# Optimization experiments

Measured on AMD Instinct MI355X. Metric: run time of the kernel, lower is better.

Reference implementation:

```python
import jax, jax.numpy as jnp
import numpy as np

N_ATOMS = 50000
N_EDGES = 400000
N_MOL = 500
HID = 128
NRBF = 20
NLAYERS = 4
N_TYPES = 100
CUTOFF = 5.0


def _xavier(key, fi, fo):
    lim = float(np.sqrt(6.0 / (fi + fo)))
    return jax.random.uniform(key, (fi, fo), minval=-lim, maxval=lim, dtype=jnp.float32)


def setup_inputs() -> dict:
    key = jax.random.key(0)
    ks = jax.random.split(key, 8)
    z = jax.random.randint(ks[0], (N_ATOMS,), 0, N_TYPES)
    pos = jax.random.normal(ks[1], (N_ATOMS, 3), dtype=jnp.float32) * 3.0
    # ensure every node receives at least one message (row covers all nodes)
    row = jnp.concatenate([jnp.arange(N_ATOMS),
                           jax.random.randint(ks[2], (N_EDGES - N_ATOMS,), 0, N_ATOMS)])
    col = jax.random.randint(ks[3], (N_EDGES,), 0, N_ATOMS)
    edge_index = jnp.stack([row, col])
    batch = jnp.sort(jax.random.randint(ks[4], (N_ATOMS,), 0, N_MOL))
    emb = jax.random.normal(ks[5], (N_TYPES, HID), dtype=jnp.float32) * 0.1
    kk = iter(jax.random.split(ks[6], 4 * NLAYERS + 4))
    filt_W1 = jnp.stack([_xavier(next(kk), NRBF, HID) for _ in range(NLAYERS)])
    filt_W2 = jnp.stack([_xavier(next(kk), HID, 3 * HID) for _ in range(NLAYERS)])
    upd_W1 = jnp.stack([_xavier(next(kk), 3 * HID, HID) for _ in range(NLAYERS)])
    upd_W2 = jnp.stack([_xavier(next(kk), HID, 3 * HID) for _ in range(NLAYERS)])
    filt_b1 = jnp.zeros((NLAYERS, HID)); filt_b2 = jnp.zeros((NLAYERS, 3 * HID))
    upd_b1 = jnp.zeros((NLAYERS, HID)); upd_b2 = jnp.zeros((NLAYERS, 3 * HID))
    lam_W1 = _xavier(next(kk), HID, HID); lam_b1 = jnp.zeros((HID,))
    lam_W2 = _xavier(next(kk), HID, 1); lam_b2 = jnp.zeros((1,))
    phi_W1 = _xavier(next(kk), HID, HID); phi_b1 = jnp.zeros((HID,))
    phi_W2 = _xavier(next(kk), HID, 1); phi_b2 = jnp.zeros((1,))
    return dict(z=z, pos=pos, edge_index=edge_index, batch=batch, emb=emb,
                filt_W1=filt_W1, filt_b1=filt_b1, filt_W2=filt_W2, filt_b2=filt_b2,
                upd_W1=upd_W1, upd_b1=upd_b1, upd_W2=upd_W2, upd_b2=upd_b2,
                lam_W1=lam_W1, lam_b1=lam_b1, lam_W2=lam_W2, lam_b2=lam_b2,
                phi_W1=phi_W1, phi_b1=phi_b1, phi_W2=phi_W2, phi_b2=phi_b2)


def reference(z, pos, edge_index, batch, emb,
              filt_W1, filt_b1, filt_W2, filt_b2,
              upd_W1, upd_b1, upd_W2, upd_b2,
              lam_W1, lam_b1, lam_W2, lam_b2,
              phi_W1, phi_b1, phi_W2, phi_b2):
    row, col = edge_index[0], edge_index[1]
    diff = pos[col] - pos[row]                      # (E,3)
    dist = jnp.linalg.norm(diff, axis=1)            # (E,)
    dirs = diff / (dist[:, None] + 1e-8)            # (E,3)
    centers = jnp.linspace(0.0, CUTOFF, NRBF)
    rbf = jnp.exp(-(dist[:, None] - centers) ** 2)  # gamma=1 buffer, (E,NRBF)

    s = emb[z]                                      # (N,H)
    v = jnp.zeros((s.shape[0], HID, 3), dtype=s.dtype)

    for i in range(NLAYERS):
        h = jax.nn.silu(rbf @ filt_W1[i] + filt_b1[i]) @ filt_W2[i] + filt_b2[i]
        phi_ss, phi_vv, phi_sv = jnp.split(h, 3, axis=-1)   # (E,H) each
        s_col = s[col]                                       # (E,H)
        m_s = phi_ss * s_col                                 # (E,H)
        m_v = phi_vv[..., None] * v[col] + (phi_sv * s_col)[..., None] * dirs[:, None, :]  # (E,H,3)
        m_s = jax.ops.segment_sum(m_s, row, num_segments=N_ATOMS)
        m_v = jax.ops.segment_sum(m_v, row, num_segments=N_ATOMS)
        v_norm = jnp.linalg.norm(m_v, axis=-1)               # (N,H)
        u = jax.nn.silu(jnp.concatenate([s, m_s, v_norm], axis=-1) @ upd_W1[i] + upd_b1[i]) @ upd_W2[i] + upd_b2[i]
        delta_s, alpha, beta = jnp.split(u, 3, axis=-1)
        s = s + delta_s
        v = alpha[..., None] * v + beta[..., None] * m_v

    h_mol = jax.ops.segment_sum(s, batch, num_segments=N_MOL)
    counts = jax.ops.segment_sum(jnp.ones((N_ATOMS,), s.dtype), batch, num_segments=N_MOL)
    h_mol = h_mol / counts[:, None]
    lam = (jax.nn.silu(h_mol @ lam_W1 + lam_b1) @ lam_W2 + lam_b2)[:, 0]
    phi = jax.nn.sigmoid(jax.nn.silu(h_mol @ phi_W1 + phi_b1) @ phi_W2 + phi_b2)[:, 0]
    return lam, phi
```

## Files before the change

kernel.cpp:

```cpp
#include <hip/hip_runtime.h>
#include <hip/hip_bf16.h>

static constexpr int NA = 50000;
static constexpr int NE = 400000;
static constexpr int HD = 128;
static constexpr int NL = 4;
static constexpr int NM = 500;
static constexpr int EPB = 32;
static constexpr int HSW = 194;

typedef __hip_bfloat16 bf16;
typedef short short8 __attribute__((ext_vector_type(8)));
typedef float float4v __attribute__((ext_vector_type(4)));

__device__ __forceinline__ unsigned short f2bf_bits(float x) {
    union { float f; unsigned int u; } c; c.f = x;
    unsigned int lsb = (c.u >> 16) & 1u;
    return (unsigned short)((c.u + 0x7fffu + lsb) >> 16);
}
__device__ __forceinline__ float bf2f(unsigned short b) {
    union { unsigned int u; float f; } c; c.u = ((unsigned int)b) << 16;
    return c.f;
}
__device__ __forceinline__ float lo16f(unsigned int u) {
    union { unsigned int x; float f; } c; c.x = u << 16; return c.f;
}
__device__ __forceinline__ float hi16f(unsigned int u) {
    union { unsigned int x; float f; } c; c.x = u & 0xffff0000u; return c.f;
}
__device__ __forceinline__ float silu_f(float x) {
    float sg = 1.0f / (1.0f + __expf(-x));
    return x * sg;
}

__global__ void geom_kernel(const float* __restrict__ pos,
                            const int* __restrict__ row, const int* __restrict__ col,
                            float* __restrict__ dist_g, float* __restrict__ dirs) {
    int e = blockIdx.x * 256 + threadIdx.x;
    if (e >= NE) return;
    int r = row[e], c = col[e];
    float dx = pos[c*3+0] - pos[r*3+0];
    float dy = pos[c*3+1] - pos[r*3+1];
    float dz = pos[c*3+2] - pos[r*3+2];
    float dist = sqrtf(dx*dx + dy*dy + dz*dz);
    float inv = 1.0f / (dist + 1e-8f);
    dist_g[e] = dist;
    dirs[e*3+0] = dx*inv; dirs[e*3+1] = dy*inv; dirs[e*3+2] = dz*inv;
}

__global__ void deg_kernel(const int* __restrict__ row, int* __restrict__ deg) {
    int e = blockIdx.x * 256 + threadIdx.x;
    if (e >= NE) return;
    atomicAdd(&deg[row[e]], 1);
}

__global__ __launch_bounds__(1024) void blockscan_kernel(const int* __restrict__ deg,
                                                         int* __restrict__ incl,
                                                         int* __restrict__ btot) {
    __shared__ int sh[1024];
    int t = threadIdx.x;
    int i = blockIdx.x * 1024 + t;
    int x = (i < NA) ? deg[i] : 0;
    sh[t] = x;
    __syncthreads();
    for (int off = 1; off < 1024; off <<= 1) {
        int v_ = (t >= off) ? sh[t - off] : 0;
        __syncthreads();
        sh[t] += v_;
        __syncthreads();
    }
    if (i < NA) incl[i] = sh[t];
    if (t == 1023) btot[blockIdx.x] = sh[t];
}

__global__ void totals_kernel(int* __restrict__ btot, int nb) {
    if (threadIdx.x == 0 && blockIdx.x == 0) {
        int acc = 0;
        for (int b = 0; b < nb; ++b) { int tv = btot[b]; btot[b] = acc; acc += tv; }
    }
}

__global__ void finalize_kernel(const int* __restrict__ deg, const int* __restrict__ incl,
                                const int* __restrict__ btot,
                                int* __restrict__ row_ptr, int* __restrict__ cursor) {
    int i = blockIdx.x * 256 + threadIdx.x;
    if (i >= NA) return;
    int inc = btot[i >> 10] + incl[i];
    row_ptr[i + 1] = inc;
    cursor[i] = inc - deg[i];
    if (i == 0) row_ptr[0] = 0;
}

__global__ void scatter_kernel(const int* __restrict__ row, int* __restrict__ cursor,
                               int* __restrict__ csr_eid) {
    int e = blockIdx.x * 256 + threadIdx.x;
    if (e >= NE) return;
    int p = atomicAdd(&cursor[row[e]], 1);
    csr_eid[p] = e;
}

__global__ void embed_kernel(const int* __restrict__ z, const float* __restrict__ emb,
                             float* __restrict__ s, uint4* __restrict__ vp2) {
    int idx = blockIdx.x * 256 + threadIdx.x;
    if (idx >= NA * 64) return;
    int n = idx >> 6, cp = idx & 63;
    float vlo = emb[z[n] * HD + cp];
    float vhi = emb[z[n] * HD + 64 + cp];
    s[(size_t)n * HD + cp] = vlo;
    s[(size_t)n * HD + 64 + cp] = vhi;
    uint4 q;
    q.x = (unsigned int)f2bf_bits(vlo);
    q.y = 0u;
    q.z = (unsigned int)f2bf_bits(vhi);
    q.w = 0u;
    vp2[idx] = q;
}

__global__ void pack_bfrag_kernel(const float* __restrict__ W, int K, int N,
                                  int layers, unsigned short* __restrict__ out) {
    int NT = N >> 4, KC = K >> 5;
    int total = layers * NT * KC * 64;
    int idx = blockIdx.x * 256 + threadIdx.x;
    if (idx >= total) return;
    int lane = idx & 63;
    int kc = (idx >> 6) % KC;
    int nt = ((idx >> 6) / KC) % NT;
    int layer = (idx >> 6) / (KC * NT);
    const float* Wl = W + (size_t)layer * K * N;
    int n = nt * 16 + (lane & 15);
    int k0 = kc * 32 + (lane >> 4) * 8;
    short8 pk;
#pragma unroll
    for (int j = 0; j < 8; ++j)
        pk[j] = (short)f2bf_bits(Wl[(size_t)(k0 + j) * N + n]);
    *(short8*)(&out[(size_t)idx * 8]) = pk;
}

__global__ void pack_w1frag_kernel(const float* __restrict__ W1all,
                                   unsigned short* __restrict__ out) {
    int idx = blockIdx.x * 256 + threadIdx.x;
    if (idx >= NL * 8 * 64) return;
    int lane = idx & 63;
    int nt = (idx >> 6) & 7;
    int layer = idx >> 9;
    const float* W1 = W1all + (size_t)layer * 20 * HD;
    int n = nt * 16 + (lane & 15);
    int k0 = (lane >> 4) * 8;
    short8 pk;
#pragma unroll
    for (int j = 0; j < 8; ++j) {
        int k = k0 + j;
        pk[j] = (k < 20) ? (short)f2bf_bits(W1[(size_t)k * HD + n]) : (short)0;
    }
    *(short8*)(&out[(size_t)idx * 8]) = pk;
}

__global__ __launch_bounds__(256, 6) void layer_msg_kernel(
    const float* __restrict__ dist_g, const int* __restrict__ csr_eid,
    const int* __restrict__ row_ptr, const int* __restrict__ row,
    const int* __restrict__ col, const float* __restrict__ dirs,
    const unsigned short* __restrict__ W1frag, const float* __restrict__ b1,
    const unsigned short* __restrict__ W2frag, const float* __restrict__ b2,
    const uint4* __restrict__ vp2,
    float* __restrict__ m_s, float* __restrict__ m_v)
{
    __shared__ __align__(16) unsigned int smem32[EPB * HSW];
    unsigned short* t_frag = (unsigned short*)smem32;
    __shared__ float dist_s[EPB];
    __shared__ int   col_s[EPB];
    __shared__ int   rid_s[EPB];
    __shared__ float dirs_s[EPB * 3];

    int tid = threadIdx.x;
    int base = blockIdx.x * EPB;

    if (tid < EPB) {
        int eid = csr_eid[base + tid];
        dist_s[tid] = dist_g[eid];
        col_s[tid] = col[eid];
        rid_s[tid] = row[eid];
        dirs_s[tid*3+0] = dirs[eid*3+0];
        dirs_s[tid*3+1] = dirs[eid*3+1];
        dirs_s[tid*3+2] = dirs[eid*3+2];
    }
    __syncthreads();

    int lane = tid & 63, w = tid >> 6;
    int colb = lane & 15, quad = lane >> 4;
    int et = w & 1, oh = w >> 1;

    {
        float d = dist_s[et * 16 + colb];
        short8 arbf;
#pragma unroll
        for (int j = 0; j < 8; ++j) {
            int k = quad * 8 + j;
            float t = d - (5.0f / 19.0f) * (float)k;
            arbf[j] = (short)f2bf_bits(__expf(-t * t));
        }
        float4v acc1[4];
#pragma unroll
        for (int nt2 = 0; nt2 < 4; ++nt2) {
            short8 b = *(const short8*)(W1frag + ((size_t)((oh * 4 + nt2) * 64 + lane)) * 8);
            float4v z = {0.f, 0.f, 0.f, 0.f};
            acc1[nt2] = __builtin_amdgcn_mfma_f32_16x16x32_bf16(arbf, b, z, 0, 0, 0);
        }
#pragma unroll
        for (int nt2 = 0; nt2 < 4; ++nt2) {
            int n1 = (oh * 4 + nt2) * 16 + colb;
            float bias = b1[n1];
            int kc2 = n1 >> 5, kq = (n1 >> 3) & 3, j2 = n1 & 7;
#pragma unroll
            for (int r = 0; r < 4; ++r) {
                float val = silu_f(acc1[nt2][r] + bias);
                int em = quad * 4 + r;
                t_frag[(((et * 4 + kc2) * 64) + kq * 16 + em) * 8 + j2] = f2bf_bits(val);
            }
        }
    }
    __syncthreads();

    short8 a[4];
#pragma unroll
    for (int kc = 0; kc < 4; ++kc)
        a[kc] = *(const short8*)(&t_frag[((et * 4 + kc) * 64 + lane) * 8]);
    __syncthreads();

    unsigned short* h16 = (unsigned short*)smem32;
    int ntb = (w >> 1) * 12;
    for (int i = 0; i < 12; ++i) {
        int nt = ntb + i;
        float4v acc = {0.f, 0.f, 0.f, 0.f};
#pragma unroll
        for (int kc = 0; kc < 4; ++kc) {
            short8 b = *(const short8*)(W2frag + ((size_t)(nt * 4 + kc) * 64 + lane) * 8);
            acc = __builtin_amdgcn_mfma_f32_16x16x32_bf16(a[kc], b, acc, 0, 0, 0);
        }
        int n = nt * 16 + colb;
        int seg = n >> 7, nch = n & 127;
        int cp = nch & 63, half = nch >> 6;
        float bias = b2[n];
        int e0 = et * 16 + quad * 4;
        unsigned short* hp = h16 + ((size_t)(e0 * HSW) + seg * 64 + cp) * 2 + half;
#pragma unroll
        for (int r = 0; r < 4; ++r)
            hp[r * HSW * 2] = f2bf_bits(acc[r] + bias);
    }
    __syncthreads();

    int cp = tid & 63, team = tid >> 6;
    const unsigned int* h32 = smem32;
    int node_lo = rid_s[0], node_hi = rid_s[EPB - 1];
    for (int n = node_lo + team; n <= node_hi; n += 4) {
        int p0 = row_ptr[n], p1 = row_ptr[n + 1];
        int lo = p0 - base; if (lo < 0) lo = 0;
        int hi = p1 - base; if (hi > EPB) hi = EPB;
        if (lo >= hi) continue;
        bool interior = (p0 >= base) && (p1 <= base + EPB);
        float as_l = 0.f, as_h = 0.f;
        float a0l = 0.f, a1l = 0.f, a2l = 0.f, a0h = 0.f, a1h = 0.f, a2h = 0.f;
        int e = lo;
        for (; e + 2 <= hi; e += 2) {
            uint4 qa = vp2[(size_t)col_s[e] * 64 + cp];
            uint4 qb = vp2[(size_t)col_s[e + 1] * 64 + cp];
#pragma unroll
            for (int j = 0; j < 2; ++j) {
                uint4 q = j ? qb : qa;
                int ee = e + j;
                unsigned int hx0 = h32[ee * HSW + cp];
                unsigned int hx1 = h32[ee * HSW + 64 + cp];
                unsigned int hx2 = h32[ee * HSW + 128 + cp];
                float d0 = dirs_s[ee*3], d1 = dirs_s[ee*3+1], d2 = dirs_s[ee*3+2];
                float sc_l = lo16f(q.x), v0_l = hi16f(q.x), v1_l = lo16f(q.y), v2_l = hi16f(q.y);
                float sc_h = lo16f(q.z), v0_h = hi16f(q.z), v1_h = lo16f(q.w), v2_h = hi16f(q.w);
                float svd_l = hi16f(hx2 << 16) * 0.f + lo16f(hx2) * sc_l;
                float svd_h = hi16f(hx2) * sc_h;
                as_l += lo16f(hx0) * sc_l;  as_h += hi16f(hx0) * sc_h;
                float pvv_l = lo16f(hx1), pvv_h = hi16f(hx1);
                a0l += pvv_l * v0_l + svd_l * d0;  a0h += pvv_h * v0_h + svd_h * d0;
                a1l += pvv_l * v1_l + svd_l * d1;  a1h += pvv_h * v1_h + svd_h * d1;
                a2l += pvv_l * v2_l + svd_l * d2;  a2h += pvv_h * v2_h + svd_h * d2;
            }
        }
        for (; e < hi; ++e) {
            uint4 q = vp2[(size_t)col_s[e] * 64 + cp];
            unsigned int hx0 = h32[e * HSW + cp];
            unsigned int hx1 = h32[e * HSW + 64 + cp];
            unsigned int hx2 = h32[e * HSW + 128 + cp];
            float d0 = dirs_s[e*3], d1 = dirs_s[e*3+1], d2 = dirs_s[e*3+2];
            float sc_l = lo16f(q.x), v0_l = hi16f(q.x), v1_l = lo16f(q.y), v2_l = hi16f(q.y);
            float sc_h = lo16f(q.z), v0_h = hi16f(q.z), v1_h = lo16f(q.w), v2_h = hi16f(q.w);
            float svd_l = lo16f(hx2) * sc_l;
            float svd_h = hi16f(hx2) * sc_h;
            as_l += lo16f(hx0) * sc_l;  as_h += hi16f(hx0) * sc_h;
            float pvv_l = lo16f(hx1), pvv_h = hi16f(hx1);
            a0l += pvv_l * v0_l + svd_l * d0;  a0h += pvv_h * v0_h + svd_h * d0;
            a1l += pvv_l * v1_l + svd_l * d1;  a1h += pvv_h * v1_h + svd_h * d1;
            a2l += pvv_l * v2_l + svd_l * d2;  a2h += pvv_h * v2_h + svd_h * d2;
        }
        size_t msx = (size_t)n * HD;
        size_t mvx = (size_t)n * 3 * HD;
        if (interior) {
            m_s[msx + cp] = as_l;          m_s[msx + 64 + cp] = as_h;
            m_v[mvx + cp] = a0l;           m_v[mvx + 64 + cp] = a0h;
            m_v[mvx + HD + cp] = a1l;      m_v[mvx + HD + 64 + cp] = a1h;
            m_v[mvx + 2*HD + cp] = a2l;    m_v[mvx + 2*HD + 64 + cp] = a2h;
        } else {
            atomicAdd(&m_s[msx + cp], as_l);          atomicAdd(&m_s[msx + 64 + cp], as_h);
            atomicAdd(&m_v[mvx + cp], a0l);           atomicAdd(&m_v[mvx + 64 + cp], a0h);
            atomicAdd(&m_v[mvx + HD + cp], a1l);      atomicAdd(&m_v[mvx + HD + 64 + cp], a1h);
            atomicAdd(&m_v[mvx + 2*HD + cp], a2l);    atomicAdd(&m_v[mvx + 2*HD + 64 + cp], a2h);
        }
    }
}

__global__ __launch_bounds__(256) void upd12_kernel(
    float* __restrict__ s, uint4* __restrict__ vp2,
    float* __restrict__ m_s, float* __restrict__ m_v,
    const unsigned short* __restrict__ W1frag, const float* __restrict__ b1,
    const unsigned short* __restrict__ W2frag, const float* __restrict__ b2)
{
    __shared__ __align__(16) unsigned short afrag[64 * 384];
    int tid = threadIdx.x;
    int r0 = blockIdx.x * 64;

#pragma unroll
    for (int t = 0; t < 12; ++t) {
        int id = tid + 256 * t;
        int r = id / 48;
        int kg = id % 48;
        int rr = r0 + r; if (rr >= NA) rr = NA - 1;
        float vals[8];
        if (kg < 16) {
            const float* p = s + (size_t)rr * HD + kg * 8;
#pragma unroll
            for (int j = 0; j < 8; ++j) vals[j] = p[j];
        } else if (kg < 32) {
            const float* p = m_s + (size_t)rr * HD + (kg - 16) * 8;
#pragma unroll
            for (int j = 0; j < 8; ++j) vals[j] = p[j];
        } else {
            int cb = (kg - 32) * 8;
            const float* p = m_v + (size_t)rr * 3 * HD + cb;
#pragma unroll
            for (int j = 0; j < 8; ++j) {
                float x = p[j], y = p[HD + j], z = p[2*HD + j];
                vals[j] = sqrtf(x*x + y*y + z*z);
            }
        }
        int kc = kg >> 2, hi = kg & 3, m = r & 15, rt = r >> 4;
        short8 pk;
#pragma unroll
        for (int j = 0; j < 8; ++j) pk[j] = (short)f2bf_bits(vals[j]);
        *(short8*)(&afrag[(((rt * 12 + kc) * 64) + hi * 16 + m) * 8]) = pk;
    }
    __syncthreads();

    int lane = tid & 63, w = tid >> 6;
    int colb = lane & 15, quad = lane >> 4;

    float4v acc1[8];
#pragma unroll
    for (int nt = 0; nt < 8; ++nt) acc1[nt] = (float4v){0.f,0.f,0.f,0.f};
    for (int kc = 0; kc < 12; ++kc) {
        short8 a = *(const short8*)(&afrag[((w * 12 + kc) * 64 + lane) * 8]);
#pragma unroll
        for (int nt = 0; nt < 8; ++nt) {
            short8 b = *(const short8*)(W1frag + ((size_t)(nt * 12 + kc) * 64 + lane) * 8);
            acc1[nt] = __builtin_amdgcn_mfma_f32_16x16x32_bf16(a, b, acc1[nt], 0, 0, 0);
        }
    }
    __syncthreads();

#pragma unroll
    for (int nt = 0; nt < 8; ++nt) {
        int n1 = nt * 16 + colb;
        int kc2 = n1 >> 5, hi2 = (n1 >> 3) & 3, j2 = n1 & 7;
#pragma unroll
        for (int r = 0; r < 4; ++r) {
            float t1v = silu_f(acc1[nt][r] + b1[n1]);
            int m2 = quad * 4 + r;
            afrag[(((w * 4 + kc2) * 64) + hi2 * 16 + m2) * 8 + j2] = f2bf_bits(t1v);
        }
    }
    __syncthreads();

    short8 a2[4];
#pragma unroll
    for (int kc = 0; kc < 4; ++kc)
        a2[kc] = *(const short8*)(&afrag[((w * 4 + kc) * 64 + lane) * 8]);

    for (int i = 0; i < 4; ++i) {
        float4v dl = {0.f,0.f,0.f,0.f}, dh = {0.f,0.f,0.f,0.f};
        float4v al = {0.f,0.f,0.f,0.f}, ah = {0.f,0.f,0.f,0.f};
        float4v bl = {0.f,0.f,0.f,0.f}, bh = {0.f,0.f,0.f,0.f};
#pragma unroll
        for (int kc = 0; kc < 4; ++kc) {
            short8 w_dl = *(const short8*)(W2frag + ((size_t)((i     ) * 4 + kc) * 64 + lane) * 8);
            short8 w_dh = *(const short8*)(W2frag + ((size_t)((i +  4) * 4 + kc) * 64 + lane) * 8);
            short8 w_al = *(const short8*)(W2frag + ((size_t)((i +  8) * 4 + kc) * 64 + lane) * 8);
            short8 w_ah = *(const short8*)(W2frag + ((size_t)((i + 12) * 4 + kc) * 64 + lane) * 8);
            short8 w_bl = *(const short8*)(W2frag + ((size_t)((i + 16) * 4 + kc) * 64 + lane) * 8);
            short8 w_bh = *(const short8*)(W2frag + ((size_t)((i + 20) * 4 + kc) * 64 + lane) * 8);
            dl = __builtin_amdgcn_mfma_f32_16x16x32_bf16(a2[kc], w_dl, dl, 0, 0, 0);
            dh = __builtin_amdgcn_mfma_f32_16x16x32_bf16(a2[kc], w_dh, dh, 0, 0, 0);
            al = __builtin_amdgcn_mfma_f32_16x16x32_bf16(a2[kc], w_al, al, 0, 0, 0);
            ah = __builtin_amdgcn_mfma_f32_16x16x32_bf16(a2[kc], w_ah, ah, 0, 0, 0);
            bl = __builtin_amdgcn_mfma_f32_16x16x32_bf16(a2[kc], w_bl, bl, 0, 0, 0);
            bh = __builtin_amdgcn_mfma_f32_16x16x32_bf16(a2[kc], w_bh, bh, 0, 0, 0);
        }
        int cp = i * 16 + colb;
        float bd_l = b2[cp],        bd_h = b2[64 + cp];
        float ba_l = b2[128 + cp],  ba_h = b2[192 + cp];
        float bb_l = b2[256 + cp],  bb_h = b2[320 + cp];
#pragma unroll
        for (int r = 0; r < 4; ++r) {
            int rr = r0 + 16 * w + quad * 4 + r;
            if (rr < NA) {
                size_t sx = (size_t)rr * HD;
                size_t vx = (size_t)rr * 3 * HD;
                float news_l = s[sx + cp]      + dl[r] + bd_l;
                float news_h = s[sx + 64 + cp] + dh[r] + bd_h;
                s[sx + cp] = news_l;
                s[sx + 64 + cp] = news_h;
                float alv_l = al[r] + ba_l, alv_h = ah[r] + ba_h;
                float bev_l = bl[r] + bb_l, bev_h = bh[r] + bb_h;
                uint4 q = vp2[(size_t)rr * 64 + cp];
                float nv0_l = alv_l * hi16f(q.x) + bev_l * m_v[vx + cp];
                float nv1_l = alv_l * lo16f(q.y) + bev_l * m_v[vx + HD + cp];
                float nv2_l = alv_l * hi16f(q.y) + bev_l * m_v[vx + 2*HD + cp];
                float nv0_h = alv_h * hi16f(q.z) + bev_h * m_v[vx + 64 + cp];
                float nv1_h = alv_h * lo16f(q.w) + bev_h * m_v[vx + HD + 64 + cp];
                float nv2_h = alv_h * hi16f(q.w) + bev_h * m_v[vx + 2*HD + 64 + cp];
                uint4 nq;
                nq.x = (unsigned int)f2bf_bits(news_l) | ((unsigned int)f2bf_bits(nv0_l) << 16);
                nq.y = (unsigned int)f2bf_bits(nv1_l)  | ((unsigned int)f2bf_bits(nv2_l) << 16);
                nq.z = (unsigned int)f2bf_bits(news_h) | ((unsigned int)f2bf_bits(nv0_h) << 16);
                nq.w = (unsigned int)f2bf_bits(nv1_h)  | ((unsigned int)f2bf_bits(nv2_h) << 16);
                vp2[(size_t)rr * 64 + cp] = nq;
                m_s[sx + cp] = 0.f;            m_s[sx + 64 + cp] = 0.f;
                m_v[vx + cp] = 0.f;            m_v[vx + 64 + cp] = 0.f;
                m_v[vx + HD + cp] = 0.f;       m_v[vx + HD + 64 + cp] = 0.f;
                m_v[vx + 2*HD + cp] = 0.f;     m_v[vx + 2*HD + 64 + cp] = 0.f;
            }
        }
    }
}

__global__ __launch_bounds__(128) void readout_kernel(
    const float* __restrict__ s, const int* __restrict__ batch,
    const float* __restrict__ lamW1, const float* __restrict__ lamb1,
    const float* __restrict__ lamW2, const float* __restrict__ lamb2,
    const float* __restrict__ phiW1, const float* __restrict__ phib1,
    const float* __restrict__ phiW2, const float* __restrict__ phib2,
    float* __restrict__ out)
{
    __shared__ int seg[2];
    __shared__ float hms[HD];
    __shared__ float red[HD];
    int m = blockIdx.x, c = threadIdx.x;
    if (c < 2) {
        int target = m + c;
        int lo = 0, hi = NA;
        while (lo < hi) { int mid = (lo + hi) >> 1; if (batch[mid] < target) lo = mid + 1; else hi = mid; }
        seg[c] = lo;
    }
    __syncthreads();
    int st = seg[0], en = seg[1];
    float acc = 0.f;
    for (int n2 = st; n2 < en; ++n2) acc += s[(size_t)n2 * HD + c];
    float hm = acc / (float)(en - st);
    hms[c] = hm;
    __syncthreads();

    float t = lamb1[c];
    for (int k = 0; k < HD; ++k) t += hms[k] * lamW1[k * HD + c];
    t = silu_f(t);
    red[c] = t * lamW2[c];
    __syncthreads();
    for (int off = 64; off > 0; off >>= 1) { if (c < off) red[c] += red[c + off]; __syncthreads(); }
    if (c == 0) out[m] = red[0] + lamb2[0];
    __syncthreads();

    t = phib1[c];
    for (int k = 0; k < HD; ++k) t += hms[k] * phiW1[k * HD + c];
    t = silu_f(t);
    red[c] = t * phiW2[c];
    __syncthreads();
    for (int off = 64; off > 0; off >>= 1) { if (c < off) red[c] += red[c + off]; __syncthreads(); }
    if (c == 0) { float x = red[0] + phib2[0]; out[NM + m] = 1.0f / (1.0f + __expf(-x)); }
}

extern "C" void kernel_launch(void* const* d_in, const int* in_sizes, int n_in,
                              void* d_out, int out_size, void* d_ws, size_t ws_size,
                              hipStream_t stream) {
    (void)in_sizes; (void)n_in; (void)out_size; (void)ws_size;
    const int*   z          = (const int*)  d_in[0];
    const float* pos        = (const float*)d_in[1];
    const int*   edge_index = (const int*)  d_in[2];
    const int*   batch      = (const int*)  d_in[3];
    const float* emb        = (const float*)d_in[4];
    const float* filt_W1    = (const float*)d_in[5];
    const float* filt_b1    = (const float*)d_in[6];
    const float* filt_W2    = (const float*)d_in[7];
    const float* filt_b2    = (const float*)d_in[8];
    const float* upd_W1     = (const float*)d_in[9];
    const float* upd_b1     = (const float*)d_in[10];
    const float* upd_W2     = (const float*)d_in[11];
    const float* upd_b2     = (const float*)d_in[12];
    const float* lam_W1     = (const float*)d_in[13];
    const float* lam_b1     = (const float*)d_in[14];
    const float* lam_W2     = (const float*)d_in[15];
    const float* lam_b2     = (const float*)d_in[16];
    const float* phi_W1     = (const float*)d_in[17];
    const float* phi_b1     = (const float*)d_in[18];
    const float* phi_W2     = (const float*)d_in[19];
    const float* phi_b2     = (const float*)d_in[20];
    float* out = (float*)d_out;

    const int* row = edge_index;
    const int* col = edge_index + NE;

    char* ws = (char*)d_ws;
    size_t off = 0;
    auto alloc = [&](size_t bytes) -> char* {
        char* p = ws + off;
        off = (off + bytes + 255) & ~(size_t)255;
        return p;
    };
    float* dist_g  = (float*)alloc((size_t)NE * 4);
    float* dirs    = (float*)alloc((size_t)NE * 3 * 4);
    int*   csr_eid = (int*)  alloc((size_t)NE * 4);
    int*   row_ptr = (int*)  alloc((size_t)(NA + 1) * 4);
    int*   deg     = (int*)  alloc((size_t)NA * 4);
    int*   cursor  = (int*)  alloc((size_t)NA * 4);
    int*   incl    = (int*)  alloc((size_t)NA * 4);
    int*   btot    = (int*)  alloc(256);
    float* s       = (float*)alloc((size_t)NA * HD * 4);
    uint4* vp2     = (uint4*)alloc((size_t)NA * 64 * 16);
    float* m_s     = (float*)alloc((size_t)NA * HD * 4);
    float* m_v     = (float*)alloc((size_t)NA * HD * 3 * 4);
    unsigned short* fW1frag = (unsigned short*)alloc((size_t)NL * 8 * 64 * 8 * 2);
    unsigned short* fW2frag = (unsigned short*)alloc((size_t)NL * 24 * 4 * 64 * 8 * 2);
    unsigned short* uW1frag = (unsigned short*)alloc((size_t)NL * 8 * 12 * 64 * 8 * 2);
    unsigned short* uW2frag = (unsigned short*)alloc((size_t)NL * 24 * 4 * 64 * 8 * 2);

    const int EB = (NE + 255) / 256;
    const int SCAN_BLOCKS = (NA + 1023) / 1024;
    const int MSG_BLOCKS = NE / EPB;
    const int UPD_BLOCKS = (NA + 63) / 64;

    hipMemsetAsync(deg, 0, (size_t)NA * 4, stream);
    hipMemsetAsync(m_s, 0, (size_t)NA * HD * 4, stream);
    hipMemsetAsync(m_v, 0, (size_t)NA * HD * 3 * 4, stream);
    geom_kernel<<<EB, 256, 0, stream>>>(pos, row, col, dist_g, dirs);
    deg_kernel<<<EB, 256, 0, stream>>>(row, deg);
    blockscan_kernel<<<SCAN_BLOCKS, 1024, 0, stream>>>(deg, incl, btot);
    totals_kernel<<<1, 64, 0, stream>>>(btot, SCAN_BLOCKS);
    finalize_kernel<<<(NA + 255) / 256, 256, 0, stream>>>(deg, incl, btot, row_ptr, cursor);
    scatter_kernel<<<EB, 256, 0, stream>>>(row, cursor, csr_eid);
    embed_kernel<<<(NA * 64 + 255) / 256, 256, 0, stream>>>(z, emb, s, vp2);
    pack_w1frag_kernel<<<8, 256, 0, stream>>>(filt_W1, fW1frag);
    pack_bfrag_kernel<<<96, 256, 0, stream>>>(filt_W2, 128, 384, NL, fW2frag);
    pack_bfrag_kernel<<<96, 256, 0, stream>>>(upd_W1, 384, 128, NL, uW1frag);
    pack_bfrag_kernel<<<96, 256, 0, stream>>>(upd_W2, 128, 384, NL, uW2frag);

    for (int i = 0; i < NL; ++i) {
        const float* fb1 = filt_b1 + (size_t)i * HD;
        const float* fb2 = filt_b2 + (size_t)i * 384;
        const unsigned short* fW1f = fW1frag + (size_t)i * 8 * 64 * 8;
        const unsigned short* fW2f = fW2frag + (size_t)i * 24 * 4 * 64 * 8;
        const unsigned short* uW1f = uW1frag + (size_t)i * 8 * 12 * 64 * 8;
        const unsigned short* uW2f = uW2frag + (size_t)i * 24 * 4 * 64 * 8;
        const float* ub1 = upd_b1 + (size_t)i * HD;
        const float* ub2 = upd_b2 + (size_t)i * 384;

        layer_msg_kernel<<<MSG_BLOCKS, 256, 0, stream>>>(
            dist_g, csr_eid, row_ptr, row, col, dirs,
            fW1f, fb1, fW2f, fb2, vp2, m_s, m_v);
        upd12_kernel<<<UPD_BLOCKS, 256, 0, stream>>>(
            s, vp2, m_s, m_v, uW1f, ub1, uW2f, ub2);
    }

    readout_kernel<<<NM, 128, 0, stream>>>(s, batch,
        lam_W1, lam_b1, lam_W2, lam_b2,
        phi_W1, phi_b1, phi_W2, phi_b2, out);
}
```

Before: 1.267 ms.

## Zero only boundary-node accumulators instead of full m_s/m_v memsets and rezeroing

Removes the full-size memsets of m_s and m_v and the per-layer zeroing stores in the update kernel. A one-time pass lists the nodes whose CSR edge ranges cross an EPB block boundary, and a small kernel zeroes only those before each message layer, because interior nodes are fully overwritten by plain stores. The message accumulation loop is also rewritten with float2 vectors so the compiler can use packed FMAs. The cost is an extra kernel launch per layer and a fixed boundary-list capacity of 16384 nodes; if more nodes cross boundaries, the overflow ones are never zeroed.

```diff
diff --git a/kernel.cpp b/kernel.cpp
--- a/kernel.cpp
+++ b/kernel.cpp
@@ -8,19 +8,17 @@
 static constexpr int NM = 500;
 static constexpr int EPB = 32;
 static constexpr int HSW = 194;
+static constexpr int BCAP = 16384;
 
 typedef __hip_bfloat16 bf16;
 typedef short short8 __attribute__((ext_vector_type(8)));
 typedef float float4v __attribute__((ext_vector_type(4)));
+typedef float float2v __attribute__((ext_vector_type(2)));
 
 __device__ __forceinline__ unsigned short f2bf_bits(float x) {
     union { float f; unsigned int u; } c; c.f = x;
     unsigned int lsb = (c.u >> 16) & 1u;
     return (unsigned short)((c.u + 0x7fffu + lsb) >> 16);
-}
-__device__ __forceinline__ float bf2f(unsigned short b) {
-    union { unsigned int u; float f; } c; c.u = ((unsigned int)b) << 16;
-    return c.f;
 }
 __device__ __forceinline__ float lo16f(unsigned int u) {
     union { unsigned int x; float f; } c; c.x = u << 16; return c.f;
@@ -97,6 +95,30 @@
     if (e >= NE) return;
     int p = atomicAdd(&cursor[row[e]], 1);
     csr_eid[p] = e;
+}
+
+__global__ void mark_boundary_kernel(const int* __restrict__ row_ptr,
+                                     int* __restrict__ blist, int* __restrict__ bcount) {
+    int n = blockIdx.x * 256 + threadIdx.x;
+    if (n >= NA) return;
+    int p0 = row_ptr[n], p1 = row_ptr[n + 1];
+    if (p0 / EPB != (p1 - 1) / EPB) {
+        int i = atomicAdd(bcount, 1);
+        if (i < BCAP) blist[i] = n;
+    }
+}
+
+__global__ void zero_boundary_kernel(const int* __restrict__ blist,
+                                     const int* __restrict__ bcount,
+                                     float* __restrict__ m_s, float* __restrict__ m_v) {
+    int idx = blockIdx.x * 256 + threadIdx.x;
+    int cnt = *bcount; if (cnt > BCAP) cnt = BCAP;
+    int ni = idx >> 7, c = idx & 127;
+    if (ni >= cnt) return;
+    int n = blist[ni];
+    m_s[(size_t)n * HD + c] = 0.f;
+    size_t vx = (size_t)n * 3 * HD + c;
+    m_v[vx] = 0.f; m_v[vx + HD] = 0.f; m_v[vx + 2*HD] = 0.f;
 }
 
 __global__ void embed_kernel(const int* __restrict__ z, const float* __restrict__ emb,
@@ -257,8 +279,7 @@
         int hi = p1 - base; if (hi > EPB) hi = EPB;
         if (lo >= hi) continue;
         bool interior = (p0 >= base) && (p1 <= base + EPB);
-        float as_l = 0.f, as_h = 0.f;
-        float a0l = 0.f, a1l = 0.f, a2l = 0.f, a0h = 0.f, a1h = 0.f, a2h = 0.f;
+        float2v as2 = {0.f, 0.f}, a02 = {0.f, 0.f}, a12 = {0.f, 0.f}, a22 = {0.f, 0.f};
         int e = lo;
         for (; e + 2 <= hi; e += 2) {
             uint4 qa = vp2[(size_t)col_s[e] * 64 + cp];
@@ -270,16 +291,19 @@
                 unsigned int hx0 = h32[ee * HSW + cp];
                 unsigned int hx1 = h32[ee * HSW + 64 + cp];
                 unsigned int hx2 = h32[ee * HSW + 128 + cp];
+                float2v sc2;  sc2.x = lo16f(q.x);   sc2.y = lo16f(q.z);
+                float2v v02;  v02.x = hi16f(q.x);   v02.y = hi16f(q.z);
+                float2v v12;  v12.x = lo16f(q.y);   v12.y = lo16f(q.w);
+                float2v v22;  v22.x = hi16f(q.y);   v22.y = hi16f(q.w);
+                float2v pss2; pss2.x = lo16f(hx0);  pss2.y = hi16f(hx0);
+                float2v pvv2; pvv2.x = lo16f(hx1);  pvv2.y = hi16f(hx1);
+                float2v psv2; psv2.x = lo16f(hx2);  psv2.y = hi16f(hx2);
+                float2v svd2 = psv2 * sc2;
+                as2 += pss2 * sc2;
                 float d0 = dirs_s[ee*3], d1 = dirs_s[ee*3+1], d2 = dirs_s[ee*3+2];
-                float sc_l = lo16f(q.x), v0_l = hi16f(q.x), v1_l = lo16f(q.y), v2_l = hi16f(q.y);
-                float sc_h = lo16f(q.z), v0_h = hi16f(q.z), v1_h = lo16f(q.w), v2_h = hi16f(q.w);
-                float svd_l = hi16f(hx2 << 16) * 0.f + lo16f(hx2) * sc_l;
-                float svd_h = hi16f(hx2) * sc_h;
-                as_l += lo16f(hx0) * sc_l;  as_h += hi16f(hx0) * sc_h;
-                float pvv_l = lo16f(hx1), pvv_h = hi16f(hx1);
-                a0l += pvv_l * v0_l + svd_l * d0;  a0h += pvv_h * v0_h + svd_h * d0;
-                a1l += pvv_l * v1_l + svd_l * d1;  a1h += pvv_h * v1_h + svd_h * d1;
-                a2l += pvv_l * v2_l + svd_l * d2;  a2h += pvv_h * v2_h + svd_h * d2;
+                a02 += pvv2 * v02 + svd2 * d0;
+                a12 += pvv2 * v12 + svd2 * d1;
+                a22 += pvv2 * v22 + svd2 * d2;
             }
         }
         for (; e < hi; ++e) {
@@ -287,36 +311,39 @@
             unsigned int hx0 = h32[e * HSW + cp];
             unsigned int hx1 = h32[e * HSW + 64 + cp];
             unsigned int hx2 = h32[e * HSW + 128 + cp];
+            float2v sc2;  sc2.x = lo16f(q.x);   sc2.y = lo16f(q.z);
+            float2v v02;  v02.x = hi16f(q.x);   v02.y = hi16f(q.z);
+            float2v v12;  v12.x = lo16f(q.y);   v12.y = lo16f(q.w);
+            float2v v22;  v22.x = hi16f(q.y);   v22.y = hi16f(q.w);
+            float2v pss2; pss2.x = lo16f(hx0);  pss2.y = hi16f(hx0);
+            float2v pvv2; pvv2.x = lo16f(hx1);  pvv2.y = hi16f(hx1);
+            float2v psv2; psv2.x = lo16f(hx2);  psv2.y = hi16f(hx2);
+            float2v svd2 = psv2 * sc2;
+            as2 += pss2 * sc2;
             float d0 = dirs_s[e*3], d1 = dirs_s[e*3+1], d2 = dirs_s[e*3+2];
-            float sc_l = lo16f(q.x), v0_l = hi16f(q.x), v1_l = lo16f(q.y), v2_l = hi16f(q.y);
-            float sc_h = lo16f(q.z), v0_h = hi16f(q.z), v1_h = lo16f(q.w), v2_h = hi16f(q.w);
-            float svd_l = lo16f(hx2) * sc_l;
-            float svd_h = hi16f(hx2) * sc_h;
-            as_l += lo16f(hx0) * sc_l;  as_h += hi16f(hx0) * sc_h;
-            float pvv_l = lo16f(hx1), pvv_h = hi16f(hx1);
-            a0l += pvv_l * v0_l + svd_l * d0;  a0h += pvv_h * v0_h + svd_h * d0;
-            a1l += pvv_l * v1_l + svd_l * d1;  a1h += pvv_h * v1_h + svd_h * d1;
-            a2l += pvv_l * v2_l + svd_l * d2;  a2h += pvv_h * v2_h + svd_h * d2;
+            a02 += pvv2 * v02 + svd2 * d0;
+            a12 += pvv2 * v12 + svd2 * d1;
+            a22 += pvv2 * v22 + svd2 * d2;
         }
         size_t msx = (size_t)n * HD;
         size_t mvx = (size_t)n * 3 * HD;
         if (interior) {
-            m_s[msx + cp] = as_l;          m_s[msx + 64 + cp] = as_h;
-            m_v[mvx + cp] = a0l;           m_v[mvx + 64 + cp] = a0h;
-            m_v[mvx + HD + cp] = a1l;      m_v[mvx + HD + 64 + cp] = a1h;
-            m_v[mvx + 2*HD + cp] = a2l;    m_v[mvx + 2*HD + 64 + cp] = a2h;
+            m_s[msx + cp] = as2.x;          m_s[msx + 64 + cp] = as2.y;
+            m_v[mvx + cp] = a02.x;          m_v[mvx + 64 + cp] = a02.y;
+            m_v[mvx + HD + cp] = a12.x;     m_v[mvx + HD + 64 + cp] = a12.y;
+            m_v[mvx + 2*HD + cp] = a22.x;   m_v[mvx + 2*HD + 64 + cp] = a22.y;
         } else {
-            atomicAdd(&m_s[msx + cp], as_l);          atomicAdd(&m_s[msx + 64 + cp], as_h);
-            atomicAdd(&m_v[mvx + cp], a0l);           atomicAdd(&m_v[mvx + 64 + cp], a0h);
-            atomicAdd(&m_v[mvx + HD + cp], a1l);      atomicAdd(&m_v[mvx + HD + 64 + cp], a1h);
-            atomicAdd(&m_v[mvx + 2*HD + cp], a2l);    atomicAdd(&m_v[mvx + 2*HD + 64 + cp], a2h);
+            atomicAdd(&m_s[msx + cp], as2.x);          atomicAdd(&m_s[msx + 64 + cp], as2.y);
+            atomicAdd(&m_v[mvx + cp], a02.x);          atomicAdd(&m_v[mvx + 64 + cp], a02.y);
+            atomicAdd(&m_v[mvx + HD + cp], a12.x);     atomicAdd(&m_v[mvx + HD + 64 + cp], a12.y);
+            atomicAdd(&m_v[mvx + 2*HD + cp], a22.x);   atomicAdd(&m_v[mvx + 2*HD + 64 + cp], a22.y);
         }
     }
 }
 
 __global__ __launch_bounds__(256) void upd12_kernel(
     float* __restrict__ s, uint4* __restrict__ vp2,
-    float* __restrict__ m_s, float* __restrict__ m_v,
+    const float* __restrict__ m_s, const float* __restrict__ m_v,
     const unsigned short* __restrict__ W1frag, const float* __restrict__ b1,
     const unsigned short* __restrict__ W2frag, const float* __restrict__ b2)
 {
@@ -438,10 +465,6 @@
                 nq.z = (unsigned int)f2bf_bits(news_h) | ((unsigned int)f2bf_bits(nv0_h) << 16);
                 nq.w = (unsigned int)f2bf_bits(nv1_h)  | ((unsigned int)f2bf_bits(nv2_h) << 16);
                 vp2[(size_t)rr * 64 + cp] = nq;
-                m_s[sx + cp] = 0.f;            m_s[sx + 64 + cp] = 0.f;
-                m_v[vx + cp] = 0.f;            m_v[vx + 64 + cp] = 0.f;
-                m_v[vx + HD + cp] = 0.f;       m_v[vx + HD + 64 + cp] = 0.f;
-                m_v[vx + 2*HD + cp] = 0.f;     m_v[vx + 2*HD + 64 + cp] = 0.f;
             }
         }
     }
@@ -536,6 +559,8 @@
     int*   cursor  = (int*)  alloc((size_t)NA * 4);
     int*   incl    = (int*)  alloc((size_t)NA * 4);
     int*   btot    = (int*)  alloc(256);
+    int*   blist   = (int*)  alloc((size_t)BCAP * 4);
+    int*   bcount  = (int*)  alloc(256);
     float* s       = (float*)alloc((size_t)NA * HD * 4);
     uint4* vp2     = (uint4*)alloc((size_t)NA * 64 * 16);
     float* m_s     = (float*)alloc((size_t)NA * HD * 4);
@@ -549,15 +574,16 @@
     const int SCAN_BLOCKS = (NA + 1023) / 1024;
     const int MSG_BLOCKS = NE / EPB;
     const int UPD_BLOCKS = (NA + 63) / 64;
+    const int ZB_BLOCKS = (BCAP * 128) / 256;
 
     hipMemsetAsync(deg, 0, (size_t)NA * 4, stream);
-    hipMemsetAsync(m_s, 0, (size_t)NA * HD * 4, stream);
-    hipMemsetAsync(m_v, 0, (size_t)NA * HD * 3 * 4, stream);
+    hipMemsetAsync(bcount, 0, 4, stream);
     geom_kernel<<<EB, 256, 0, stream>>>(pos, row, col, dist_g, dirs);
     deg_kernel<<<EB, 256, 0, stream>>>(row, deg);
     blockscan_kernel<<<SCAN_BLOCKS, 1024, 0, stream>>>(deg, incl, btot);
     totals_kernel<<<1, 64, 0, stream>>>(btot, SCAN_BLOCKS);
     finalize_kernel<<<(NA + 255) / 256, 256, 0, stream>>>(deg, incl, btot, row_ptr, cursor);
+    mark_boundary_kernel<<<(NA + 255) / 256, 256, 0, stream>>>(row_ptr, blist, bcount);
     scatter_kernel<<<EB, 256, 0, stream>>>(row, cursor, csr_eid);
     embed_kernel<<<(NA * 64 + 255) / 256, 256, 0, stream>>>(z, emb, s, vp2);
     pack_w1frag_kernel<<<8, 256, 0, stream>>>(filt_W1, fW1frag);
@@ -575,6 +601,7 @@
         const float* ub1 = upd_b1 + (size_t)i * HD;
         const float* ub2 = upd_b2 + (size_t)i * 384;
 
+        zero_boundary_kernel<<<ZB_BLOCKS, 256, 0, stream>>>(blist, bcount, m_s, m_v);
         layer_msg_kernel<<<MSG_BLOCKS, 256, 0, stream>>>(
             dist_g, csr_eid, row_ptr, row, col, dirs,
             fW1f, fb1, fW2f, fb2, vp2, m_s, m_v);
```

After: 1.236 ms. -2.5%, faster.
